# Optimization experiments

Hardware: AMD Instinct MI355X
Metric: run time of the kernel (lower is better)

The kernel has to match this reference:

```python
import jax, jax.numpy as jnp
import numpy as np

SEQ, BATCH, HIDDEN = 4096, 16, 512


def setup_inputs() -> dict:
    key = jax.random.key(0)
    ks = jax.random.split(key, 8)
    scale = 1.0 / np.sqrt(HIDDEN)
    outputs_hidden = jax.random.normal(ks[0], (1, BATCH, HIDDEN), jnp.float32)
    encoder_out = jax.random.normal(ks[1], (SEQ, BATCH, HIDDEN), jnp.float32)
    encoder_features = jax.random.normal(ks[2], (SEQ, BATCH, HIDDEN), jnp.float32)
    # binary-ish float mask, mostly ones
    encoder_mask = (jax.random.uniform(ks[3], (BATCH, 1, SEQ)) > 0.1).astype(jnp.float32)
    # running sum of positive exp-scores; keep strictly positive
    temporal_scores_sum = jax.random.uniform(ks[4], (BATCH, 1, SEQ)) + 0.5
    W_feat = jax.random.normal(ks[5], (HIDDEN, HIDDEN), jnp.float32) * scale
    b_feat = jax.random.normal(ks[6], (HIDDEN,), jnp.float32)
    v_attn = jax.random.normal(ks[7], (HIDDEN,), jnp.float32) * scale
    return {
        "outputs_hidden": outputs_hidden,
        "encoder_out": encoder_out,
        "encoder_features": encoder_features,
        "encoder_mask": encoder_mask,
        "temporal_scores_sum": temporal_scores_sum,
        "W_feat": W_feat,
        "b_feat": b_feat,
        "v_attn": v_attn,
    }


def reference(outputs_hidden, encoder_out, encoder_features, encoder_mask,
              temporal_scores_sum, W_feat, b_feat, v_attn):
    # self.features: Linear(hidden, hidden) on decoder state [1, b, h]
    decoder_features = jnp.einsum('obh,kh->obk', outputs_hidden, W_feat) + b_feat
    # additive score: tanh(dec + enc) . v  -> [s, b]
    scores = jnp.einsum('sbh,h->sb', jnp.tanh(decoder_features + encoder_features), v_attn)
    # Permute(1,2,0) of [s,b,1] -> [b,1,s], then exp
    temporal_attention = jnp.exp(scores).T[:, None, :]  # [b, 1, s]
    attention = temporal_attention / temporal_scores_sum
    new_scores_sum = temporal_attention + temporal_scores_sum
    attention = attention * encoder_mask
    attention = attention / jnp.sum(attention, axis=-1, keepdims=True)  # Normalize(-1)
    enc = jnp.transpose(encoder_out, (1, 0, 2))           # [b, s, h]
    context = jnp.matmul(attention, enc)                  # [b, 1, h]
    context = jnp.transpose(context, (1, 0, 2))           # [1, b, h]
    return context, attention, new_scores_sum
```

## Files before the change

### kernel.cpp

```cpp
#include <hip/hip_runtime.h>
#include <hip/hip_bf16.h>
#include <stdint.h>

#define SEQ 4096
#define BATCH 16
#define HID 512
#define ATT_OFF (BATCH * HID)
#define NSS_OFF (BATCH * HID + BATCH * SEQ)
#define SPB 32
#define NCHUNK (SEQ / SPB)
#define SPW (SPB / 4)

typedef unsigned short u16;
typedef unsigned int u32;

__device__ __forceinline__ float bflo(u32 w) { return __uint_as_float(w << 16); }
__device__ __forceinline__ float bfhi(u32 w) { return __uint_as_float(w & 0xffff0000u); }

__device__ __forceinline__ u16 f2bf(float f) {
  u32 u = __float_as_uint(f);
  return (u16)((u + 0x7fffu + ((u >> 16) & 1u)) >> 16);
}

__device__ __forceinline__ int probe_bf16(const void* tssp) {
  const u16* t = (const u16*)tssp;
  int ok = 1;
  #pragma unroll
  for (int i = 0; i < 8; i += 2) {
    u16 u = t[i];
    ok &= (u >= 0x3F00 && u <= 0x3FC0) ? 1 : 0;
  }
  return ok;
}

template <int BF>
__device__ __forceinline__ float ld1(const void* p, size_t i) {
  if (BF) return __uint_as_float(((u32)((const u16*)p)[i]) << 16);
  return ((const float*)p)[i];
}

template <int BF>
__device__ __forceinline__ void st1(void* p, size_t i, float v) {
  if (BF) ((u16*)p)[i] = f2bf(v);
  else    ((float*)p)[i] = v;
}

template <int BF>
__device__ __forceinline__ void load8(const void* p, size_t e, float* o) {
  if (BF) {
    uint4 v = *(const uint4*)((const u16*)p + e);
    o[0]=bflo(v.x); o[1]=bfhi(v.x); o[2]=bflo(v.y); o[3]=bfhi(v.y);
    o[4]=bflo(v.z); o[5]=bfhi(v.z); o[6]=bflo(v.w); o[7]=bfhi(v.w);
  } else {
    const float4* f = (const float4*)((const float*)p + e);
    float4 a = f[0], b = f[1];
    o[0]=a.x; o[1]=a.y; o[2]=a.z; o[3]=a.w;
    o[4]=b.x; o[5]=b.y; o[6]=b.z; o[7]=b.w;
  }
}

__device__ __forceinline__ float fast_tanh(float x) {
  float e = __expf(2.0f * x);
  return 1.0f - 2.0f * __builtin_amdgcn_rcpf(e + 1.0f);
}

template <int BF>
__device__ __forceinline__ void k_dec_body(
    const void* oh, const void* W, const void* bias, float* dec) {
  int tid = threadIdx.x;
  int gw = blockIdx.x * 4 + (tid >> 6);
  int lane = tid & 63;
  int k = gw & (HID - 1);
  int b = gw >> 9;
  float wv[8], ov[8];
  load8<BF>(W,  (size_t)k * HID + lane * 8, wv);
  load8<BF>(oh, (size_t)b * HID + lane * 8, ov);
  float acc = 0.0f;
  #pragma unroll
  for (int j = 0; j < 8; ++j) acc += wv[j] * ov[j];
  #pragma unroll
  for (int off = 32; off; off >>= 1) acc += __shfl_xor(acc, off, 64);
  if (lane == 0) dec[b * HID + k] = acc + ld1<BF>(bias, k);
}

__global__ __launch_bounds__(256) void k_dec(
    const void* oh, const void* W, const void* bias, const void* tss,
    float* dec, float* denom) {
  if (blockIdx.x == 0 && threadIdx.x < BATCH) denom[threadIdx.x] = 0.0f;
  if (probe_bf16(tss)) k_dec_body<1>(oh, W, bias, dec);
  else                 k_dec_body<0>(oh, W, bias, dec);
}

template <int BF>
__device__ __forceinline__ void k_fused_body(
    const void* ef, const void* eo, const void* maskp, const void* tssp,
    const void* vp, const float* dec, float* w_buf, float* denom,
    float* partial, void* out) {
  int tid = threadIdx.x, lane = tid & 63, wave = tid >> 6;
  int blk = blockIdx.x;
  int b = blk >> 7;
  int chunk = blk & (NCHUNK - 1);
  int s0 = chunk * SPB + wave * SPW;
  float dv[8], vv[8];
  #pragma unroll
  for (int j = 0; j < 8; ++j) dv[j] = dec[b * HID + lane * 8 + j];
  load8<BF>(vp, lane * 8, vv);

  float acc[SPW];
  #pragma unroll
  for (int i = 0; i < SPW; ++i) {
    float ev[8];
    load8<BF>(ef, ((size_t)(s0 + i) * BATCH + b) * HID + lane * 8, ev);
    float s = 0.0f;
    #pragma unroll
    for (int j = 0; j < 8; ++j) s += fast_tanh(ev[j] + dv[j]) * vv[j];
    acc[i] = s;
  }
  #pragma unroll
  for (int off = 32; off; off >>= 1) {
    #pragma unroll
    for (int i = 0; i < SPW; ++i) acc[i] += __shfl_xor(acc[i], off, 64);
  }
  float w[SPW];
  float wsum = 0.0f;
  #pragma unroll
  for (int i = 0; i < SPW; ++i) {
    int s = s0 + i;
    float p  = __expf(acc[i]);
    float ts = ld1<BF>(tssp,  b * SEQ + s);
    float m  = ld1<BF>(maskp, b * SEQ + s);
    w[i] = p * m * __builtin_amdgcn_rcpf(ts);
    wsum += w[i];
    if (lane == 0) {
      st1<BF>(out, NSS_OFF + b * SEQ + s, p + ts);
      w_buf[b * SEQ + s] = w[i];
    }
  }
  float a[8] = {0,0,0,0,0,0,0,0};
  #pragma unroll
  for (int i = 0; i < SPW; ++i) {
    float eov[8];
    load8<BF>(eo, ((size_t)(s0 + i) * BATCH + b) * HID + lane * 8, eov);
    #pragma unroll
    for (int j = 0; j < 8; ++j) a[j] += w[i] * eov[j];
  }
  __shared__ float red[3 * 8 * 64];
  __shared__ float wpart[4];
  if (lane == 0) wpart[wave] = wsum;
  if (wave > 0) {
    #pragma unroll
    for (int j = 0; j < 8; ++j) red[((wave - 1) * 8 + j) * 64 + lane] = a[j];
  }
  __syncthreads();
  if (wave == 0) {
    #pragma unroll
    for (int k = 0; k < 3; ++k)
      #pragma unroll
      for (int j = 0; j < 8; ++j) a[j] += red[(k * 8 + j) * 64 + lane];
    float4* p4 = (float4*)(partial + ((size_t)b * NCHUNK + chunk) * HID + lane * 8);
    p4[0] = make_float4(a[0], a[1], a[2], a[3]);
    p4[1] = make_float4(a[4], a[5], a[6], a[7]);
    if (tid == 0)
      atomicAdd(&denom[b], wpart[0] + wpart[1] + wpart[2] + wpart[3]);
  }
}

__global__ __launch_bounds__(256) void k_fused(
    const void* ef, const void* eo, const void* maskp, const void* tssp,
    const void* vp, const float* dec, float* w_buf, float* denom,
    float* partial, void* out) {
  if (probe_bf16(tssp))
    k_fused_body<1>(ef, eo, maskp, tssp, vp, dec, w_buf, denom, partial, out);
  else
    k_fused_body<0>(ef, eo, maskp, tssp, vp, dec, w_buf, denom, partial, out);
}

template <int BF>
__device__ __forceinline__ void k_fin_body(
    const float* w_buf, const float* denom, const float* partial, void* out) {
  int b = blockIdx.x >> 3;
  int part = blockIdx.x & 7;
  int tid = threadIdx.x;
  float inv_d = __builtin_amdgcn_rcpf(denom[b]);
  #pragma unroll
  for (int k = 0; k < 2; ++k) {
    int s = part * 512 + k * 256 + tid;
    st1<BF>(out, ATT_OFF + b * SEQ + s, w_buf[b * SEQ + s] * inv_d);
  }
  if (tid < 64) {
    int h = part * 64 + tid;
    float sum = 0.0f;
    for (int c = 0; c < NCHUNK; ++c)
      sum += partial[((size_t)b * NCHUNK + c) * HID + h];
    st1<BF>(out, b * HID + h, sum * inv_d);
  }
}

__global__ __launch_bounds__(256) void k_finalize(
    const float* w_buf, const float* denom, const float* partial,
    const void* tssp, void* out) {
  if (probe_bf16(tssp)) k_fin_body<1>(w_buf, denom, partial, out);
  else                  k_fin_body<0>(w_buf, denom, partial, out);
}

extern "C" void kernel_launch(void* const* d_in, const int* in_sizes, int n_in,
                              void* d_out, int out_size, void* d_ws, size_t ws_size,
                              hipStream_t stream) {
  const void* oh   = d_in[0];
  const void* eo   = d_in[1];
  const void* ef   = d_in[2];
  const void* mask = d_in[3];
  const void* tss  = d_in[4];
  const void* W    = d_in[5];
  const void* bias = d_in[6];
  const void* v    = d_in[7];

  float* ws      = (float*)d_ws;
  float* dec     = ws;
  float* w_buf   = dec + BATCH * HID;
  float* denom   = w_buf + BATCH * SEQ;
  float* partial = denom + 16;

  k_dec     <<<2048, 256, 0, stream>>>(oh, W, bias, tss, dec, denom);
  k_fused   <<<2048, 256, 0, stream>>>(ef, eo, mask, tss, v, dec, w_buf,
                                       denom, partial, d_out);
  k_finalize<<< 128, 256, 0, stream>>>(w_buf, denom, partial, tss, d_out);
}
```

Measured before the change: 303.4 us.

## Split fused kernel into scores and context kernels with batched loads

New measurement: 305.9 us. Within noise of the previous version (+0.8%).

```diff
diff --git a/kernel.cpp b/kernel.cpp
--- a/kernel.cpp
+++ b/kernel.cpp
@@ -92,15 +92,20 @@
 }
 
 template <int BF>
-__device__ __forceinline__ void k_fused_body(
-    const void* ef, const void* eo, const void* maskp, const void* tssp,
-    const void* vp, const float* dec, float* w_buf, float* denom,
-    float* partial, void* out) {
+__device__ __forceinline__ void k_scores_body(
+    const void* ef, const void* maskp, const void* tssp, const void* vp,
+    const float* dec, float* w_buf, float* denom, void* out) {
   int tid = threadIdx.x, lane = tid & 63, wave = tid >> 6;
   int blk = blockIdx.x;
-  int b = blk >> 7;
-  int chunk = blk & (NCHUNK - 1);
+  int b = blk & (BATCH - 1);
+  int chunk = blk >> 4;
   int s0 = chunk * SPB + wave * SPW;
+
+  float ev[SPW][8];
+  #pragma unroll
+  for (int i = 0; i < SPW; ++i)
+    load8<BF>(ef, ((size_t)(s0 + i) * BATCH + b) * HID + lane * 8, ev[i]);
+
   float dv[8], vv[8];
   #pragma unroll
   for (int j = 0; j < 8; ++j) dv[j] = dec[b * HID + lane * 8 + j];
@@ -109,11 +114,9 @@
   float acc[SPW];
   #pragma unroll
   for (int i = 0; i < SPW; ++i) {
-    float ev[8];
-    load8<BF>(ef, ((size_t)(s0 + i) * BATCH + b) * HID + lane * 8, ev);
     float s = 0.0f;
     #pragma unroll
-    for (int j = 0; j < 8; ++j) s += fast_tanh(ev[j] + dv[j]) * vv[j];
+    for (int j = 0; j < 8; ++j) s += fast_tanh(ev[i][j] + dv[j]) * vv[j];
     acc[i] = s;
   }
   #pragma unroll
@@ -121,7 +124,6 @@
     #pragma unroll
     for (int i = 0; i < SPW; ++i) acc[i] += __shfl_xor(acc[i], off, 64);
   }
-  float w[SPW];
   float wsum = 0.0f;
   #pragma unroll
   for (int i = 0; i < SPW; ++i) {
@@ -129,24 +131,54 @@
     float p  = __expf(acc[i]);
     float ts = ld1<BF>(tssp,  b * SEQ + s);
     float m  = ld1<BF>(maskp, b * SEQ + s);
-    w[i] = p * m * __builtin_amdgcn_rcpf(ts);
-    wsum += w[i];
+    float wv = p * m * __builtin_amdgcn_rcpf(ts);
+    wsum += wv;
     if (lane == 0) {
       st1<BF>(out, NSS_OFF + b * SEQ + s, p + ts);
-      w_buf[b * SEQ + s] = w[i];
+      w_buf[b * SEQ + s] = wv;
     }
   }
-  float a[8] = {0,0,0,0,0,0,0,0};
-  #pragma unroll
-  for (int i = 0; i < SPW; ++i) {
-    float eov[8];
-    load8<BF>(eo, ((size_t)(s0 + i) * BATCH + b) * HID + lane * 8, eov);
-    #pragma unroll
-    for (int j = 0; j < 8; ++j) a[j] += w[i] * eov[j];
-  }
-  __shared__ float red[3 * 8 * 64];
   __shared__ float wpart[4];
   if (lane == 0) wpart[wave] = wsum;
+  __syncthreads();
+  if (tid == 0)
+    atomicAdd(&denom[b], wpart[0] + wpart[1] + wpart[2] + wpart[3]);
+}
+
+__global__ __launch_bounds__(256, 4) void k_scores(
+    const void* ef, const void* maskp, const void* tssp, const void* vp,
+    const float* dec, float* w_buf, float* denom, void* out) {
+  if (probe_bf16(tssp))
+    k_scores_body<1>(ef, maskp, tssp, vp, dec, w_buf, denom, out);
+  else
+    k_scores_body<0>(ef, maskp, tssp, vp, dec, w_buf, denom, out);
+}
+
+template <int BF>
+__device__ __forceinline__ void k_ctx_body(
+    const void* eo, const float* w_buf, float* partial) {
+  int tid = threadIdx.x, lane = tid & 63, wave = tid >> 6;
+  int blk = blockIdx.x;
+  int b = blk & (BATCH - 1);
+  int chunk = blk >> 4;
+  int s0 = chunk * SPB + wave * SPW;
+
+  float eov[SPW][8];
+  #pragma unroll
+  for (int i = 0; i < SPW; ++i)
+    load8<BF>(eo, ((size_t)(s0 + i) * BATCH + b) * HID + lane * 8, eov[i]);
+
+  float w[SPW];
+  #pragma unroll
+  for (int i = 0; i < SPW; ++i) w[i] = w_buf[b * SEQ + s0 + i];
+
+  float a[8] = {0,0,0,0,0,0,0,0};
+  #pragma unroll
+  for (int i = 0; i < SPW; ++i)
+    #pragma unroll
+    for (int j = 0; j < 8; ++j) a[j] += w[i] * eov[i][j];
+
+  __shared__ float red[3 * 8 * 64];
   if (wave > 0) {
     #pragma unroll
     for (int j = 0; j < 8; ++j) red[((wave - 1) * 8 + j) * 64 + lane] = a[j];
@@ -160,40 +192,35 @@
     float4* p4 = (float4*)(partial + ((size_t)b * NCHUNK + chunk) * HID + lane * 8);
     p4[0] = make_float4(a[0], a[1], a[2], a[3]);
     p4[1] = make_float4(a[4], a[5], a[6], a[7]);
-    if (tid == 0)
-      atomicAdd(&denom[b], wpart[0] + wpart[1] + wpart[2] + wpart[3]);
-  }
-}
-
-__global__ __launch_bounds__(256) void k_fused(
-    const void* ef, const void* eo, const void* maskp, const void* tssp,
-    const void* vp, const float* dec, float* w_buf, float* denom,
-    float* partial, void* out) {
-  if (probe_bf16(tssp))
-    k_fused_body<1>(ef, eo, maskp, tssp, vp, dec, w_buf, denom, partial, out);
-  else
-    k_fused_body<0>(ef, eo, maskp, tssp, vp, dec, w_buf, denom, partial, out);
+  }
+}
+
+__global__ __launch_bounds__(256, 4) void k_ctx(
+    const void* eo, const void* tssp, const float* w_buf, float* partial) {
+  if (probe_bf16(tssp)) k_ctx_body<1>(eo, w_buf, partial);
+  else                  k_ctx_body<0>(eo, w_buf, partial);
 }
 
 template <int BF>
 __device__ __forceinline__ void k_fin_body(
     const float* w_buf, const float* denom, const float* partial, void* out) {
-  int b = blockIdx.x >> 3;
-  int part = blockIdx.x & 7;
-  int tid = threadIdx.x;
+  int b = blockIdx.x >> 5;
+  int part = blockIdx.x & 31;
+  int t = threadIdx.x;
   float inv_d = __builtin_amdgcn_rcpf(denom[b]);
-  #pragma unroll
-  for (int k = 0; k < 2; ++k) {
-    int s = part * 512 + k * 256 + tid;
+  if (t < 128) {
+    int s = part * 128 + t;
     st1<BF>(out, ATT_OFF + b * SEQ + s, w_buf[b * SEQ + s] * inv_d);
   }
-  if (tid < 64) {
-    int h = part * 64 + tid;
-    float sum = 0.0f;
-    for (int c = 0; c < NCHUNK; ++c)
-      sum += partial[((size_t)b * NCHUNK + c) * HID + h];
-    st1<BF>(out, b * HID + h, sum * inv_d);
-  }
+  int hl = t >> 4, cp = t & 15;
+  int h = part * 16 + hl;
+  float sum = 0.0f;
+  #pragma unroll
+  for (int c = cp; c < NCHUNK; c += 16)
+    sum += partial[((size_t)b * NCHUNK + c) * HID + h];
+  #pragma unroll
+  for (int off = 8; off; off >>= 1) sum += __shfl_xor(sum, off, 64);
+  if (cp == 0) st1<BF>(out, b * HID + h, sum * inv_d);
 }
 
 __global__ __launch_bounds__(256) void k_finalize(
@@ -222,7 +249,7 @@
   float* partial = denom + 16;
 
   k_dec     <<<2048, 256, 0, stream>>>(oh, W, bias, tss, dec, denom);
-  k_fused   <<<2048, 256, 0, stream>>>(ef, eo, mask, tss, v, dec, w_buf,
-                                       denom, partial, d_out);
-  k_finalize<<< 128, 256, 0, stream>>>(w_buf, denom, partial, tss, d_out);
-}
+  k_scores  <<<2048, 256, 0, stream>>>(ef, mask, tss, v, dec, w_buf, denom, d_out);
+  k_ctx     <<<2048, 256, 0, stream>>>(eo, tss, w_buf, partial);
+  k_finalize<<< 512, 256, 0, stream>>>(w_buf, denom, partial, tss, d_out);
+}
```
